# Kernel tuning notes

Hardware: AMD Instinct MI355X
Metric: run time of the kernel (lower is better)

The kernel has to match this reference:

```python
import jax, jax.numpy as jnp
import numpy as np

GROUP_SIZE = 128
EPS = 1e-6
# AWQ nibble interleave order within each int32
_AWQ_SHIFTS = jnp.array([0, 4, 1, 5, 2, 6, 3, 7], dtype=jnp.uint32) * 4


def dequant_awq(qw, qz, sc, group_size=GROUP_SIZE):
    # qw: (in, out//8) int32, qz: (in//g, out//8) int32, sc: (in//g, out) float
    in_dim = qw.shape[0]
    w4 = ((qw.astype(jnp.uint32)[:, :, None] >> _AWQ_SHIFTS) & 0xF).astype(sc.dtype)
    z4 = ((qz.astype(jnp.uint32)[:, :, None] >> _AWQ_SHIFTS) & 0xF).astype(sc.dtype)
    w4 = w4.reshape(in_dim, -1)                    # (in, out)
    z4 = z4.reshape(qz.shape[0], -1)               # (in//g, out)
    z = jnp.repeat(z4, group_size, axis=0)         # (in, out)
    s = jnp.repeat(sc, group_size, axis=0)         # (in, out)
    return (w4 - z) * s


def rmsnorm(x, w, eps=EPS):
    return x * w * jax.lax.rsqrt(jnp.mean(x * x, axis=-1, keepdims=True) + eps)


def setup_inputs() -> dict:
    key = jax.random.key(0)
    ks = jax.random.split(key, 16)
    H, I, G = 2048, 8192, GROUP_SIZE
    IMAX = 2**31 - 1
    d = {}
    d['x'] = jax.random.normal(ks[0], (2, 2048, H), dtype=jnp.float32)
    d['ln1_w'] = jnp.ones((H,), jnp.float32)
    d['ln2_w'] = jnp.ones((H,), jnp.float32)
    d['qkv_qw'] = jax.random.randint(ks[1], (H, 3 * H // 8), 0, IMAX, dtype=jnp.int32)
    d['qkv_qz'] = jax.random.randint(ks[2], (H // G, 3 * H // 8), 0, IMAX, dtype=jnp.int32)
    d['qkv_sc'] = jax.random.normal(ks[3], (H // G, 3 * H), dtype=jnp.float32) * 0.02
    d['o_qw'] = jax.random.randint(ks[4], (H, H // 8), 0, IMAX, dtype=jnp.int32)
    d['o_qz'] = jax.random.randint(ks[5], (H // G, H // 8), 0, IMAX, dtype=jnp.int32)
    d['o_sc'] = jax.random.normal(ks[6], (H // G, H), dtype=jnp.float32) * 0.02
    d['gu_qw'] = jax.random.randint(ks[7], (H, 2 * I // 8), 0, IMAX, dtype=jnp.int32)
    d['gu_qz'] = jax.random.randint(ks[8], (H // G, 2 * I // 8), 0, IMAX, dtype=jnp.int32)
    d['gu_sc'] = jax.random.normal(ks[9], (H // G, 2 * I), dtype=jnp.float32) * 0.02
    d['dn_qw'] = jax.random.randint(ks[10], (I, H // 8), 0, IMAX, dtype=jnp.int32)
    d['dn_qz'] = jax.random.randint(ks[11], (I // G, H // 8), 0, IMAX, dtype=jnp.int32)
    d['dn_sc'] = jax.random.normal(ks[12], (I // G, H), dtype=jnp.float32) * 0.02
    return d


def reference(x, ln1_w, ln2_w, qkv_qw, qkv_qz, qkv_sc, o_qw, o_qz, o_sc,
              gu_qw, gu_qz, gu_sc, dn_qw, dn_qz, dn_sc):
    H = x.shape[-1]
    # attention-ish block (mock: qkv proj, take q slice, o proj)
    residual = x
    h = rmsnorm(x, ln1_w)
    qkv = h @ dequant_awq(qkv_qw, qkv_qz, qkv_sc)          # (..., 3H)
    q = qkv[..., :H]
    o = q @ dequant_awq(o_qw, o_qz, o_sc)                  # (..., H)
    x = residual + o
    # SwiGLU MLP
    residual = x
    h = rmsnorm(x, ln2_w)
    gate_up = h @ dequant_awq(gu_qw, gu_qz, gu_sc)         # (..., 2I)
    gate, up = jnp.split(gate_up, 2, axis=-1)
    mlp = (jax.nn.silu(gate) * up) @ dequant_awq(dn_qw, dn_qz, dn_sc)
    return residual + mlp
```

## Files before the change

kernel.cpp:

```cpp
#include <hip/hip_runtime.h>
#include <hip/hip_bf16.h>
#include <stdint.h>

typedef __bf16 bf16x8 __attribute__((ext_vector_type(8)));
typedef __bf16 bf16x2 __attribute__((ext_vector_type(2)));
typedef float  f32x4  __attribute__((ext_vector_type(4)));

template <int V> struct ic { static constexpr int value = V; };

__device__ __forceinline__ void gload_lds16(const void* g, void* l) {
  __builtin_amdgcn_global_load_lds(
      (const __attribute__((address_space(1))) void*)g,
      (__attribute__((address_space(3))) void*)l, 16, 0, 0);
}

__global__ __launch_bounds__(256) void rmsnorm_kernel(
    const float* __restrict__ x, const float* __restrict__ w,
    __bf16* __restrict__ out) {
  constexpr int H = 2048;
  const int row = blockIdx.x;
  const int t = threadIdx.x;
  const float4* xr = (const float4*)(x + (size_t)row * H);
  float4 a = xr[t * 2 + 0];
  float4 b = xr[t * 2 + 1];
  float ss = a.x*a.x + a.y*a.y + a.z*a.z + a.w*a.w
           + b.x*b.x + b.y*b.y + b.z*b.z + b.w*b.w;
#pragma unroll
  for (int o = 32; o > 0; o >>= 1) ss += __shfl_xor(ss, o);
  __shared__ float red[4];
  if ((t & 63) == 0) red[t >> 6] = ss;
  __syncthreads();
  float tot = red[0] + red[1] + red[2] + red[3];
  float r = rsqrtf(tot * (1.0f / H) + 1e-6f);
  const float4* wr4 = (const float4*)w;
  float4 wa = wr4[t * 2 + 0];
  float4 wb = wr4[t * 2 + 1];
  bf16x8 ov;
  ov[0] = (__bf16)(a.x * wa.x * r);
  ov[1] = (__bf16)(a.y * wa.y * r);
  ov[2] = (__bf16)(a.z * wa.z * r);
  ov[3] = (__bf16)(a.w * wa.w * r);
  ov[4] = (__bf16)(b.x * wb.x * r);
  ov[5] = (__bf16)(b.y * wb.y * r);
  ov[6] = (__bf16)(b.z * wb.z * r);
  ov[7] = (__bf16)(b.w * wb.w * r);
  *(bf16x8*)(out + (size_t)row * H + (size_t)t * 8) = ov;
}

template <int GU>
__global__ __launch_bounds__(256) void dequant_t_kernel(
    const int* __restrict__ qw, const int* __restrict__ qz,
    const float* __restrict__ sc, __bf16* __restrict__ wt,
    int K, int Cp, int Nfull) {
  const int t = threadIdx.x;
  const int k0 = blockIdx.x * 128 + (t & 63) * 2;
  const int c0 = blockIdx.y * 64 + (t >> 6) * 16;
  const int g = k0 >> 7;
  const uint32_t* qw0 = (const uint32_t*)qw + (size_t)k0 * Cp + c0;
  const uint32_t* qw1 = qw0 + Cp;
  const uint32_t* qzr = (const uint32_t*)qz + (size_t)g * Cp + c0;
  const float* scr = sc + (size_t)g * Nfull + (size_t)c0 * 8;

  uint32_t u0[16], u1[16], z[16];
#pragma unroll
  for (int j = 0; j < 4; j++) {
    *(int4*)(&u0[j*4]) = *(const int4*)(qw0 + j*4);
    *(int4*)(&u1[j*4]) = *(const int4*)(qw1 + j*4);
    *(int4*)(&z[j*4])  = *(const int4*)(qzr + j*4);
  }

#pragma unroll
  for (int i = 0; i < 16; i++) {
#pragma unroll
    for (int s = 0; s < 8; s++) {
      const int sh = ((s >> 1) * 4) + ((s & 1) ? 16 : 0);
      const float zf = (float)((z[i] >> sh) & 15u);
      const float scv = scr[i * 8 + s];
      const float w0 = ((float)((u0[i] >> sh) & 15u) - zf) * scv;
      const float w1 = ((float)((u1[i] >> sh) & 15u) - zf) * scv;
      const int n = (c0 + i) * 8 + s;
      int row;
      if (GU) row = (n < 8192) ? ((n >> 4) * 32 + (n & 15))
                               : (((n - 8192) >> 4) * 32 + 16 + (n & 15));
      else    row = n;
      bf16x2 pv = {(__bf16)w0, (__bf16)w1};
      *(bf16x2*)(wt + (size_t)row * K + k0) = pv;
    }
  }
}

template <int BN, int EPI, int KC>
__global__ __launch_bounds__(512, 2) void gemm8p_kernel(
    const __bf16* __restrict__ A, const __bf16* __restrict__ Bt,
    void* __restrict__ Cv, const float* __restrict__ addend,
    int M, int N) {
  constexpr int NT = KC / 64;
  constexpr int BQ = BN / 64;
  constexpr int NSTRIP = BN / 4;
  constexpr int NI = NSTRIP / 16;

  __shared__ alignas(16) __bf16 As[8 * 4096];
  __shared__ alignas(16) __bf16 Bs[2 * BQ * 4096];

  const int t = threadIdx.x;
  const int w = t >> 6, l = t & 63;
  const int lm = l & 15, kb = l >> 4;
  const int l7 = lm & 7;
  const int wm = w >> 2, wn = w & 3;

  const size_t stat = (size_t)(t >> 3) * KC + (size_t)(((t & 7) ^ ((t >> 3) & 7)) << 3);

  const int nwg = gridDim.x;
  const int bid = blockIdx.x;
  const int swz = (bid & 7) * (nwg >> 3) + (bid >> 3);
  const int nbm = M >> 8;
  const int per_g = nbm * 8;
  const int grp = swz / per_g, v = swz % per_g;
  const int bm0 = (v % nbm) * 256;
  const int bn0 = (grp * 8 + v / nbm) * BN;

  const __bf16* Ab = A + (size_t)bm0 * KC;
  const __bf16* Bb = Bt + (size_t)bn0 * KC;

  const uint32_t gsw0 = (uint32_t)((kb ^ l7) << 4);
  const uint32_t gsw1 = (uint32_t)(((4 + kb) ^ l7) << 4);
  const uint32_t arow = (uint32_t)(wm * 16384 + lm * 128);
  const uint32_t aoff0 = arow + gsw0, aoff1 = arow + gsw1;
  const uint32_t brow = (BN == 256)
      ? (uint32_t)(wn * 8192 + lm * 128)
      : (uint32_t)((wn >> 1) * 8192 + (wn & 1) * 4096 + lm * 128);
  const uint32_t boff0 = brow + gsw0, boff1 = brow + gsw1;
  const char* AsC = (const char*)As;
  const char* BsC = (const char*)Bs;

#pragma unroll
  for (int qa = 0; qa < 4; ++qa)
    gload_lds16(Ab + stat + (size_t)(qa * 64) * KC, As + qa * 4096 + t * 8);
#pragma unroll
  for (int qb = 0; qb < BQ; ++qb)
    gload_lds16(Bb + stat + (size_t)(qb * 64) * KC, Bs + qb * 4096 + t * 8);
#pragma unroll
  for (int qb = 0; qb < BQ; ++qb)
    gload_lds16(Bb + stat + (size_t)(qb * 64) * KC + 64, Bs + (BQ + qb) * 4096 + t * 8);
  gload_lds16(Ab + stat + 64, As + 4 * 4096 + t * 8);
  gload_lds16(Ab + stat + (size_t)128 * KC + 64, As + 6 * 4096 + t * 8);
  if (BN == 256) asm volatile("s_waitcnt vmcnt(6)" ::: "memory");
  else           asm volatile("s_waitcnt vmcnt(4)" ::: "memory");
  __builtin_amdgcn_s_barrier();

  const __bf16* pA0 = Ab + stat + 128;
  const __bf16* pA1 = Ab + stat + (size_t)64 * KC + 64;
  const __bf16* pA2 = Ab + stat + (size_t)128 * KC + 128;
  const __bf16* pA3 = Ab + stat + (size_t)192 * KC + 64;
  const __bf16* pB0 = Bb + stat + 128;
  const __bf16* pB1 = Bb + stat + (size_t)64 * KC + 128;
  const __bf16* pB2 = Bb + stat + (size_t)128 * KC + 128;
  const __bf16* pB3 = Bb + stat + (size_t)192 * KC + 128;

  f32x4 acc[8][NI] = {};
  bf16x8 bfr[NI][2];

  auto tile = [&](auto Dc, auto Sc) {
    constexpr int D = decltype(Dc)::value;
    constexpr int STG = decltype(Sc)::value;
#pragma unroll
    for (int q = 0; q < 4; ++q) {
      bf16x8 af[2][2];
#pragma unroll
      for (int m2 = 0; m2 < 2; ++m2) {
        const int mi = q * 2 + m2;
        const uint32_t imA = (uint32_t)((D * 4 + (mi >> 2)) * 8192 + (mi & 3) * 2048);
        af[m2][0] = *(const bf16x8*)(AsC + aoff0 + imA);
        af[m2][1] = *(const bf16x8*)(AsC + aoff1 + imA);
      }
      if (q == 0) {
#pragma unroll
        for (int ni = 0; ni < NI; ++ni) {
          const uint32_t imB = (uint32_t)(D * BQ * 8192 + ni * 2048);
          bfr[ni][0] = *(const bf16x8*)(BsC + boff0 + imB);
          bfr[ni][1] = *(const bf16x8*)(BsC + boff1 + imB);
        }
      }
      if (STG >= 1 && q == 0) {
        gload_lds16(pA1, As + ((D ^ 1) * 4 + 1) * 4096 + t * 8);
        gload_lds16(pA3, As + ((D ^ 1) * 4 + 3) * 4096 + t * 8);
      }
      if (STG == 2) {
        if (q == 1) {
          gload_lds16(pB0, Bs + (D * BQ + 0) * 4096 + t * 8);
          gload_lds16(pB1, Bs + (D * BQ + 1) * 4096 + t * 8);
        }
        if (q == 2) {
          if (BN == 256) {
            gload_lds16(pB2, Bs + (D * BQ + 2) * 4096 + t * 8);
            gload_lds16(pB3, Bs + (D * BQ + 3) * 4096 + t * 8);
          } else {
            gload_lds16(pA0, As + (D * 4 + 0) * 4096 + t * 8);
            gload_lds16(pA2, As + (D * 4 + 2) * 4096 + t * 8);
          }
        }
        if (BN == 256 && q == 3) {
          gload_lds16(pA0, As + (D * 4 + 0) * 4096 + t * 8);
          gload_lds16(pA2, As + (D * 4 + 2) * 4096 + t * 8);
        }
      }
      __builtin_amdgcn_s_barrier();
      __builtin_amdgcn_s_setprio(1);
#pragma unroll
      for (int kk = 0; kk < 2; ++kk)
#pragma unroll
        for (int ni = 0; ni < NI; ++ni)
#pragma unroll
          for (int m2 = 0; m2 < 2; ++m2)
            acc[q * 2 + m2][ni] = __builtin_amdgcn_mfma_f32_16x16x32_bf16(
                af[m2][kk], bfr[ni][kk], acc[q * 2 + m2][ni], 0, 0, 0);
      __builtin_amdgcn_s_setprio(0);
      if (q == 3) {
        if (STG == 2) {
          if (BN == 256) asm volatile("s_waitcnt vmcnt(6)" ::: "memory");
          else           asm volatile("s_waitcnt vmcnt(4)" ::: "memory");
        } else if (STG == 1) {
          asm volatile("s_waitcnt vmcnt(0)" ::: "memory");
        }
      }
      __builtin_amdgcn_s_barrier();
    }
    if (STG == 2) {
      pA0 += 64; pA1 += 64; pA2 += 64; pA3 += 64;
      pB0 += 64; pB1 += 64;
      if (BN == 256) { pB2 += 64; pB3 += 64; }
    }
  };

#pragma unroll 1
  for (int it = 0; it < NT / 2 - 1; ++it) {
    tile(ic<0>{}, ic<2>{});
    tile(ic<1>{}, ic<2>{});
  }
  tile(ic<0>{}, ic<1>{});
  tile(ic<1>{}, ic<0>{});

  const int crow0 = bm0 + wm * 128;
#pragma unroll
  for (int mi = 0; mi < 8; ++mi) {
    if (EPI == 2) {
#pragma unroll
      for (int p = 0; p < NI / 2; ++p) {
        const int ni = p * 2;
        const int col = ((bn0 + wn * 64 + ni * 16) >> 5) * 16 + lm;
#pragma unroll
        for (int r = 0; r < 4; ++r) {
          const int row = crow0 + mi * 16 + kb * 4 + r;
          const float gv = acc[mi][ni][r], uv = acc[mi][ni + 1][r];
          const float av = uv * (gv / (1.0f + __expf(-gv)));
          ((__bf16*)Cv)[(size_t)row * 8192 + col] = (__bf16)av;
        }
      }
    } else {
#pragma unroll
      for (int ni = 0; ni < NI; ++ni) {
        const int col = bn0 + wn * NSTRIP + ni * 16 + lm;
#pragma unroll
        for (int r = 0; r < 4; ++r) {
          const int row = crow0 + mi * 16 + kb * 4 + r;
          const size_t idx = (size_t)row * N + col;
          if (EPI == 0) ((__bf16*)Cv)[idx] = (__bf16)acc[mi][ni][r];
          else          ((float*)Cv)[idx] = addend[idx] + acc[mi][ni][r];
        }
      }
    }
  }
}

extern "C" void kernel_launch(void* const* d_in, const int* in_sizes, int n_in,
                              void* d_out, int out_size, void* d_ws, size_t ws_size,
                              hipStream_t stream) {
  const float* x      = (const float*)d_in[0];
  const float* ln1    = (const float*)d_in[1];
  const float* ln2    = (const float*)d_in[2];
  const int*   qkv_qw = (const int*)d_in[3];
  const int*   qkv_qz = (const int*)d_in[4];
  const float* qkv_sc = (const float*)d_in[5];
  const int*   o_qw   = (const int*)d_in[6];
  const int*   o_qz   = (const int*)d_in[7];
  const float* o_sc   = (const float*)d_in[8];
  const int*   gu_qw  = (const int*)d_in[9];
  const int*   gu_qz  = (const int*)d_in[10];
  const float* gu_sc  = (const float*)d_in[11];
  const int*   dn_qw  = (const int*)d_in[12];
  const int*   dn_qz  = (const int*)d_in[13];
  const float* dn_sc  = (const float*)d_in[14];

  constexpr int M = 4096;

  char* ws = (char*)d_ws;
  __bf16* h   = (__bf16*)(ws + 0);
  __bf16* q   = (__bf16*)(ws + 16777216ULL);
  float*  x2  = (float*)(ws + 33554432ULL);
  __bf16* W   = (__bf16*)(ws + 67108864ULL);
  __bf16* act = (__bf16*)(ws + 134217728ULL);
  __bf16* Wdn = (__bf16*)(ws + 0);

  rmsnorm_kernel<<<dim3(M), dim3(256), 0, stream>>>(x, ln1, h);
  dequant_t_kernel<0><<<dim3(16, 4), dim3(256), 0, stream>>>(qkv_qw, qkv_qz, qkv_sc, W, 2048, 768, 6144);
  gemm8p_kernel<128, 0, 2048><<<dim3(256), dim3(512), 0, stream>>>(h, W, (void*)q, nullptr, M, 2048);
  dequant_t_kernel<0><<<dim3(16, 4), dim3(256), 0, stream>>>(o_qw, o_qz, o_sc, W, 2048, 256, 2048);
  gemm8p_kernel<128, 1, 2048><<<dim3(256), dim3(512), 0, stream>>>(q, W, (void*)x2, x, M, 2048);
  rmsnorm_kernel<<<dim3(M), dim3(256), 0, stream>>>(x2, ln2, h);
  dequant_t_kernel<1><<<dim3(16, 32), dim3(256), 0, stream>>>(gu_qw, gu_qz, gu_sc, W, 2048, 2048, 16384);
  gemm8p_kernel<256, 2, 2048><<<dim3(1024), dim3(512), 0, stream>>>(h, W, (void*)act, nullptr, M, 16384);
  dequant_t_kernel<0><<<dim3(64, 4), dim3(256), 0, stream>>>(dn_qw, dn_qz, dn_sc, Wdn, 8192, 256, 2048);
  gemm8p_kernel<128, 1, 8192><<<dim3(256), dim3(512), 0, stream>>>(act, Wdn, d_out, x2, M, 2048);
}
```

Measured before the change: 556.2 us.

## Software-pipeline LDS fragment loads one quarter ahead of MFMA in GEMM loop

Restructures the GEMM inner tile into a ping-pong register pipeline. A-fragments for the next quarter, and B-fragments for the next K tile, are read from LDS while the current quarter's MFMAs run. This targets the stall where each quarter waited on its LDS reads before issuing matrix ops. It doubles the fragment registers, which raises register pressure and could cut occupancy, and it reorders the vmcnt waits and barriers.

```diff
diff --git a/kernel.cpp b/kernel.cpp
--- a/kernel.cpp
+++ b/kernel.cpp
@@ -133,6 +133,36 @@
   const char* AsC = (const char*)As;
   const char* BsC = (const char*)Bs;
 
+  f32x4 acc[8][NI] = {};
+  bf16x8 af[2][2][2];
+  bf16x8 bfr[2][NI][2];
+
+  auto ldAf = [&](int dD, int mi, bf16x8* dst) {
+    const uint32_t imA = (uint32_t)((dD * 4 + (mi >> 2)) * 8192 + (mi & 3) * 2048);
+    dst[0] = *(const bf16x8*)(AsC + aoff0 + imA);
+    dst[1] = *(const bf16x8*)(AsC + aoff1 + imA);
+  };
+  auto ldBf = [&](int dD) {
+#pragma unroll
+    for (int ni = 0; ni < NI; ++ni) {
+      const uint32_t imB = (uint32_t)(dD * BQ * 8192 + ni * 2048);
+      bfr[dD][ni][0] = *(const bf16x8*)(BsC + boff0 + imB);
+      bfr[dD][ni][1] = *(const bf16x8*)(BsC + boff1 + imB);
+    }
+  };
+  auto mfma4 = [&](int q, bf16x8 afq[2][2], int dD) {
+    __builtin_amdgcn_s_setprio(1);
+#pragma unroll
+    for (int kk = 0; kk < 2; ++kk)
+#pragma unroll
+      for (int ni = 0; ni < NI; ++ni)
+#pragma unroll
+        for (int m2 = 0; m2 < 2; ++m2)
+          acc[q * 2 + m2][ni] = __builtin_amdgcn_mfma_f32_16x16x32_bf16(
+              afq[m2][kk], bfr[dD][ni][kk], acc[q * 2 + m2][ni], 0, 0, 0);
+    __builtin_amdgcn_s_setprio(0);
+  };
+
 #pragma unroll
   for (int qa = 0; qa < 4; ++qa)
     gload_lds16(Ab + stat + (size_t)(qa * 64) * KC, As + qa * 4096 + t * 8);
@@ -147,6 +177,10 @@
   if (BN == 256) asm volatile("s_waitcnt vmcnt(6)" ::: "memory");
   else           asm volatile("s_waitcnt vmcnt(4)" ::: "memory");
   __builtin_amdgcn_s_barrier();
+
+  ldAf(0, 0, af[0][0]); ldAf(0, 1, af[0][1]);
+  ldBf(0);
+  asm volatile("" ::: "memory");
 
   const __bf16* pA0 = Ab + stat + 128;
   const __bf16* pA1 = Ab + stat + (size_t)64 * KC + 64;
@@ -157,74 +191,58 @@
   const __bf16* pB2 = Bb + stat + (size_t)128 * KC + 128;
   const __bf16* pB3 = Bb + stat + (size_t)192 * KC + 128;
 
-  f32x4 acc[8][NI] = {};
-  bf16x8 bfr[NI][2];
-
   auto tile = [&](auto Dc, auto Sc) {
     constexpr int D = decltype(Dc)::value;
     constexpr int STG = decltype(Sc)::value;
-#pragma unroll
-    for (int q = 0; q < 4; ++q) {
-      bf16x8 af[2][2];
-#pragma unroll
-      for (int m2 = 0; m2 < 2; ++m2) {
-        const int mi = q * 2 + m2;
-        const uint32_t imA = (uint32_t)((D * 4 + (mi >> 2)) * 8192 + (mi & 3) * 2048);
-        af[m2][0] = *(const bf16x8*)(AsC + aoff0 + imA);
-        af[m2][1] = *(const bf16x8*)(AsC + aoff1 + imA);
+    ldAf(D, 2, af[1][0]); ldAf(D, 3, af[1][1]);
+    asm volatile("" ::: "memory");
+    if (STG >= 1) {
+      gload_lds16(pA1, As + ((D ^ 1) * 4 + 1) * 4096 + t * 8);
+      gload_lds16(pA3, As + ((D ^ 1) * 4 + 3) * 4096 + t * 8);
+    }
+    __builtin_amdgcn_s_barrier();
+    mfma4(0, af[0], D);
+    __builtin_amdgcn_s_barrier();
+    ldAf(D, 4, af[0][0]); ldAf(D, 5, af[0][1]);
+    asm volatile("" ::: "memory");
+    if (STG == 2) {
+      gload_lds16(pB0, Bs + (D * BQ + 0) * 4096 + t * 8);
+      gload_lds16(pB1, Bs + (D * BQ + 1) * 4096 + t * 8);
+    }
+    __builtin_amdgcn_s_barrier();
+    mfma4(1, af[1], D);
+    __builtin_amdgcn_s_barrier();
+    ldAf(D, 6, af[1][0]); ldAf(D, 7, af[1][1]);
+    asm volatile("" ::: "memory");
+    if (STG == 2) {
+      if (BN == 256) {
+        gload_lds16(pB2, Bs + (D * BQ + 2) * 4096 + t * 8);
+        gload_lds16(pB3, Bs + (D * BQ + 3) * 4096 + t * 8);
+      } else {
+        gload_lds16(pA0, As + (D * 4 + 0) * 4096 + t * 8);
+        gload_lds16(pA2, As + (D * 4 + 2) * 4096 + t * 8);
       }
-      if (q == 0) {
-#pragma unroll
-        for (int ni = 0; ni < NI; ++ni) {
-          const uint32_t imB = (uint32_t)(D * BQ * 8192 + ni * 2048);
-          bfr[ni][0] = *(const bf16x8*)(BsC + boff0 + imB);
-          bfr[ni][1] = *(const bf16x8*)(BsC + boff1 + imB);
-        }
-      }
-      if (STG >= 1 && q == 0) {
-        gload_lds16(pA1, As + ((D ^ 1) * 4 + 1) * 4096 + t * 8);
-        gload_lds16(pA3, As + ((D ^ 1) * 4 + 3) * 4096 + t * 8);
-      }
-      if (STG == 2) {
-        if (q == 1) {
-          gload_lds16(pB0, Bs + (D * BQ + 0) * 4096 + t * 8);
-          gload_lds16(pB1, Bs + (D * BQ + 1) * 4096 + t * 8);
-        }
-        if (q == 2) {
-          if (BN == 256) {
-            gload_lds16(pB2, Bs + (D * BQ + 2) * 4096 + t * 8);
-            gload_lds16(pB3, Bs + (D * BQ + 3) * 4096 + t * 8);
-          } else {
-            gload_lds16(pA0, As + (D * 4 + 0) * 4096 + t * 8);
-            gload_lds16(pA2, As + (D * 4 + 2) * 4096 + t * 8);
-          }
-        }
-        if (BN == 256 && q == 3) {
-          gload_lds16(pA0, As + (D * 4 + 0) * 4096 + t * 8);
-          gload_lds16(pA2, As + (D * 4 + 2) * 4096 + t * 8);
-        }
-      }
-      __builtin_amdgcn_s_barrier();
-      __builtin_amdgcn_s_setprio(1);
-#pragma unroll
-      for (int kk = 0; kk < 2; ++kk)
-#pragma unroll
-        for (int ni = 0; ni < NI; ++ni)
-#pragma unroll
-          for (int m2 = 0; m2 < 2; ++m2)
-            acc[q * 2 + m2][ni] = __builtin_amdgcn_mfma_f32_16x16x32_bf16(
-                af[m2][kk], bfr[ni][kk], acc[q * 2 + m2][ni], 0, 0, 0);
-      __builtin_amdgcn_s_setprio(0);
-      if (q == 3) {
-        if (STG == 2) {
-          if (BN == 256) asm volatile("s_waitcnt vmcnt(6)" ::: "memory");
-          else           asm volatile("s_waitcnt vmcnt(4)" ::: "memory");
-        } else if (STG == 1) {
-          asm volatile("s_waitcnt vmcnt(0)" ::: "memory");
-        }
-      }
-      __builtin_amdgcn_s_barrier();
-    }
+    }
+    __builtin_amdgcn_s_barrier();
+    mfma4(2, af[0], D);
+    __builtin_amdgcn_s_barrier();
+    asm volatile("s_waitcnt lgkmcnt(0)" ::: "memory");
+    __builtin_amdgcn_sched_barrier(0);
+    if (STG == 2)      asm volatile("s_waitcnt vmcnt(4)" ::: "memory");
+    else if (STG == 1) asm volatile("s_waitcnt vmcnt(0)" ::: "memory");
+    __builtin_amdgcn_s_barrier();
+    if (STG >= 1) {
+      ldAf(D ^ 1, 0, af[0][0]); ldAf(D ^ 1, 1, af[0][1]);
+      ldBf(D ^ 1);
+      asm volatile("" ::: "memory");
+    }
+    if (STG == 2 && BN == 256) {
+      gload_lds16(pA0, As + (D * 4 + 0) * 4096 + t * 8);
+      gload_lds16(pA2, As + (D * 4 + 2) * 4096 + t * 8);
+    }
+    __builtin_amdgcn_sched_barrier(0);
+    mfma4(3, af[1], D);
+    __builtin_amdgcn_s_barrier();
     if (STG == 2) {
       pA0 += 64; pA1 += 64; pA2 += 64; pA3 += 64;
       pB0 += 64; pB1 += 64;
```

Result: faster. 513.4 us (-7.7%).
